# Optimization experiments

Measured on AMD Instinct MI355X. Metric: run time of the kernel, lower is better.

## Reference

```python
import jax, jax.numpy as jnp
import numpy as np

IMG_SIZE = 640
NUM_CLASSES = 80
KA = 3
STRIDES = (8, 16, 32)
CONF_THRESH = 0.001
NMS_THRESH = 0.6
ANCHORS = np.array([[12, 16], [19, 36], [40, 28],
                    [36, 75], [76, 55], [72, 146],
                    [142, 110], [192, 243], [459, 401]], np.float32).reshape(3, 3, 2)
CLS_OFFSET = 4.0  # > max normalized coord (1.0); separates classes for class-wise NMS


def _make_grid(stride):
    f = IMG_SIZE // stride
    gy, gx = jnp.meshgrid(jnp.arange(f), jnp.arange(f), indexing='ij')
    # [HW, 1, 2] in (x, y) order, row-major over (H, W) like permute(1,2,0).view(-1,...)
    return jnp.stack([gx, gy], axis=-1).reshape(-1, 1, 2).astype(jnp.float32)


def _decode_level(pred, level):
    # pred: [KA*(1+C+4), H, W] -> obj [HW*KA,1], cls [HW*KA,C], boxes [HW*KA,4]
    C = NUM_CLASSES
    p = jnp.transpose(pred, (1, 2, 0)).reshape(-1, KA * (1 + C + 4))  # [HW, ch]
    obj = p[:, :KA].reshape(-1, 1)
    cls = p[:, KA:KA * (1 + C)].reshape(-1, C)
    reg = p[:, KA * (1 + C):].reshape(-1, KA, 4)
    grid = _make_grid(STRIDES[level])               # [HW, 1, 2]
    anchors = jnp.asarray(ANCHORS[level])           # [KA, 2]
    xy = (jax.nn.sigmoid(reg[..., :2]) + grid) * STRIDES[level]
    wh = jnp.exp(reg[..., 2:]) * anchors
    box = jnp.concatenate([xy - wh * 0.5, xy + wh * 0.5], axis=-1).reshape(-1, 4)
    return obj, cls, box


def _greedy_nms(boxes, scores, valid, thresh):
    # Faithful sequential greedy NMS (same math as the numpy loop), via lax.scan.
    N = boxes.shape[0]
    order = jnp.argsort(-scores)
    b = boxes[order]
    v = valid[order]
    areas = (b[:, 2] - b[:, 0]) * (b[:, 3] - b[:, 1])
    idx = jnp.arange(N)

    def step(suppressed, i):
        keep_i = v[i] & jnp.logical_not(suppressed[i])
        xx1 = jnp.maximum(b[i, 0], b[:, 0])
        yy1 = jnp.maximum(b[i, 1], b[:, 1])
        xx2 = jnp.minimum(b[i, 2], b[:, 2])
        yy2 = jnp.minimum(b[i, 3], b[:, 3])
        w = jnp.maximum(1e-28, xx2 - xx1)
        h = jnp.maximum(1e-28, yy2 - yy1)
        inter = w * h
        ovr = inter / (areas[i] + areas - inter + 1e-14)
        suppressed = suppressed | (keep_i & (ovr > thresh) & (idx > i))
        return suppressed, keep_i

    _, kept_sorted = jax.lax.scan(step, jnp.zeros(N, bool), idx)
    return jnp.zeros(N, bool).at[order].set(kept_sorted)


def _forward(pred_s, pred_m, pred_l):
    outs = [_decode_level(p, i) for i, p in enumerate((pred_s, pred_m, pred_l))]
    obj = jnp.concatenate([o[0] for o in outs], axis=0)   # [N, 1]
    cls = jnp.concatenate([o[1] for o in outs], axis=0)   # [N, C]
    box = jnp.concatenate([o[2] for o in outs], axis=0)   # [N, 4]
    bboxes = jnp.clip(box / IMG_SIZE, 0.0, 1.0)
    scores = jax.nn.sigmoid(obj) * jax.nn.softmax(cls, axis=-1)  # [N, C]
    cls_inds = jnp.argmax(scores, axis=1)
    conf = jnp.max(scores, axis=1)
    valid = conf >= CONF_THRESH
    # per-class NMS == class-offset trick: different classes never overlap
    nms_boxes = bboxes + cls_inds.astype(bboxes.dtype)[:, None] * CLS_OFFSET
    keep = _greedy_nms(jax.lax.stop_gradient(nms_boxes),
                       jax.lax.stop_gradient(conf), valid, NMS_THRESH)
    return bboxes, conf, cls_inds, keep


def setup_inputs() -> dict:
    key = jax.random.key(0)
    k1, k2, k3 = jax.random.split(key, 3)
    ch = KA * (1 + NUM_CLASSES + 4)  # 255
    return {
        'pred_s': jax.random.normal(k1, (ch, 80, 80), jnp.float32),
        'pred_m': jax.random.normal(k2, (ch, 40, 40), jnp.float32),
        'pred_l': jax.random.normal(k3, (ch, 20, 20), jnp.float32),
    }


def reference(pred_s, pred_m, pred_l):
    # returns fixed-shape (bboxes [N,4], scores [N], cls_inds [N], keep mask [N])
    return _forward(pred_s, pred_m, pred_l)
```

## Files before the change

### kernel.cpp

```cpp
#include <hip/hip_runtime.h>

typedef unsigned long long u64;
typedef unsigned int u32;

#define N_TOT 25200
#define NCLS 80
#define CAP 512

__device__ __constant__ float c_AW[9] = {12.f,19.f,40.f,36.f,76.f,72.f,142.f,192.f,459.f};
__device__ __constant__ float c_AH[9] = {16.f,36.f,28.f,75.f,55.f,146.f,110.f,243.f,401.f};

__global__ __launch_bounds__(64)
void decode_kernel(const float* __restrict__ p0,
                   const float* __restrict__ p1,
                   const float* __restrict__ p2,
                   float* __restrict__ out)
{
    const int m = blockIdx.x * 64 + threadIdx.x;
    if (m >= N_TOT) return;

    const float* p; int f, strd, base, ml;
    int lvl;
    if (m < 19200)      { p = p0; f = 80; strd = 8;  base = 0;     lvl = 0; ml = m; }
    else if (m < 24000) { p = p1; f = 40; strd = 16; base = 19200; lvl = 1; ml = m - 19200; }
    else                { p = p2; f = 20; strd = 32; base = 24000; lvl = 2; ml = m - 24000; }
    const int HW = f * f;
    const int a  = ml / HW;
    const int hw = ml - a * HW;
    const int gx = hw % f;
    const int gy = hw / f;
    const float* cell = p + hw;

    const float* clsp = cell + (3 + a * NCLS) * HW;
    float v[80];
    #pragma unroll
    for (int c = 0; c < 80; ++c) v[c] = clsp[c * HW];
    const float obj = cell[a * HW];
    const float* regp = cell + (243 + a * 4) * HW;
    const float tx = regp[0];
    const float ty = regp[HW];
    const float tw = regp[2 * HW];
    const float th = regp[3 * HW];

    float gm = v[0];
    #pragma unroll
    for (int c = 1; c < 80; ++c) gm = fmaxf(gm, v[c]);
    float gs = 0.f, bp = -1.f; int ba_ = 0;
    #pragma unroll
    for (int c = 0; c < 80; ++c) {
        const float pc = expf(v[c] - gm);
        gs += pc;
        if (pc > bp) { bp = pc; ba_ = c; }
    }

    const float sig  = 1.f / (1.f + expf(-obj));
    const float conf = sig * (bp / gs);
    const int n = base + hw * 3 + a;

    const float sx = 1.f / (1.f + expf(-tx));
    const float sy = 1.f / (1.f + expf(-ty));
    const float cx = (sx + (float)gx) * (float)strd;
    const float cy = (sy + (float)gy) * (float)strd;
    const int ai = lvl * 3 + a;
    const float w  = expf(tw) * c_AW[ai];
    const float h  = expf(th) * c_AH[ai];
    const float hx = w * 0.5f, hy = h * 0.5f;
    float x1 = (cx - hx) / 640.0f;
    float y1 = (cy - hy) / 640.0f;
    float x2 = (cx + hx) / 640.0f;
    float y2 = (cy + hy) / 640.0f;
    x1 = fminf(fmaxf(x1, 0.f), 1.f);
    y1 = fminf(fmaxf(y1, 0.f), 1.f);
    x2 = fminf(fmaxf(x2, 0.f), 1.f);
    y2 = fminf(fmaxf(y2, 0.f), 1.f);

    *(float4*)(out + n * 4) = make_float4(x1, y1, x2, y2);
    out[100800 + n] = conf;
    out[126000 + n] = (float)ba_;
    out[151200 + n] = 0.0f;
}

__global__ __launch_bounds__(1024)
void nms_kernel(const float* __restrict__ out,
                float* __restrict__ out_keep)
{
    const int c = blockIdx.x;
    const int tid = threadIdx.x;
    const int wave = tid >> 6, lane = tid & 63;

    __shared__ int    scnt;
    __shared__ u64    skey[CAP];
    __shared__ float4 sbox[CAP + 1];
    __shared__ int    sgi[CAP];
    __shared__ u64    maskT[8 * CAP];

    if (tid == 0) scnt = 0;
    __syncthreads();

    const float* confp = out + 100800;
    const float* clsp  = out + 126000;
    float4 cf[7], cl[7];
    bool   inb[7];
    #pragma unroll
    for (int itr = 0; itr < 7; ++itr) {
        const int ib = itr * 1024 + tid;
        inb[itr] = (ib < 6300);
        if (inb[itr]) {
            cf[itr] = *(const float4*)(confp + ib * 4);
            cl[itr] = *(const float4*)(clsp  + ib * 4);
        } else {
            cf[itr] = make_float4(-1.f, -1.f, -1.f, -1.f);
            cl[itr] = make_float4(0.f, 0.f, 0.f, 0.f);
        }
    }
    const u64 lt = (1ull << lane) - 1ull;
    #pragma unroll
    for (int itr = 0; itr < 7; ++itr) {
        const bool m0 = inb[itr] && ((int)cl[itr].x == c) && (cf[itr].x >= 0.001f);
        const bool m1 = inb[itr] && ((int)cl[itr].y == c) && (cf[itr].y >= 0.001f);
        const bool m2 = inb[itr] && ((int)cl[itr].z == c) && (cf[itr].z >= 0.001f);
        const bool m3 = inb[itr] && ((int)cl[itr].w == c) && (cf[itr].w >= 0.001f);
        const u64 b0 = __ballot(m0), b1 = __ballot(m1), b2 = __ballot(m2), b3 = __ballot(m3);
        const int t0 = __popcll(b0), t1 = __popcll(b1), t2 = __popcll(b2), t3 = __popcll(b3);
        const int tot = t0 + t1 + t2 + t3;
        if (tot) {
            int bs = 0;
            if (lane == 0) bs = atomicAdd(&scnt, tot);
            bs = __shfl(bs, 0);
            const int i0 = itr * 4096 + tid * 4;
            int pos;
            if (m0) { pos = bs + __popcll(b0 & lt);
                      if (pos < CAP) skey[pos] = ((u64)__float_as_uint(cf[itr].x) << 32) | (u64)(~(u32)(i0)); }
            if (m1) { pos = bs + t0 + __popcll(b1 & lt);
                      if (pos < CAP) skey[pos] = ((u64)__float_as_uint(cf[itr].y) << 32) | (u64)(~(u32)(i0 + 1)); }
            if (m2) { pos = bs + t0 + t1 + __popcll(b2 & lt);
                      if (pos < CAP) skey[pos] = ((u64)__float_as_uint(cf[itr].z) << 32) | (u64)(~(u32)(i0 + 2)); }
            if (m3) { pos = bs + t0 + t1 + t2 + __popcll(b3 & lt);
                      if (pos < CAP) skey[pos] = ((u64)__float_as_uint(cf[itr].w) << 32) | (u64)(~(u32)(i0 + 3)); }
        }
    }
    __syncthreads();
    const int M  = min(scnt, CAP);
    const int MW = (M + 63) >> 6;

    if (wave < MW) {
        const int e = (wave << 6) + lane;
        if (e < M) {
            const u64 ke = skey[e];
            int rank = 0;
            int j = 0;
            for (; j + 16 <= M; j += 16) {
                rank += (int)(skey[j]    > ke) + (int)(skey[j+1]  > ke)
                      + (int)(skey[j+2]  > ke) + (int)(skey[j+3]  > ke)
                      + (int)(skey[j+4]  > ke) + (int)(skey[j+5]  > ke)
                      + (int)(skey[j+6]  > ke) + (int)(skey[j+7]  > ke)
                      + (int)(skey[j+8]  > ke) + (int)(skey[j+9]  > ke)
                      + (int)(skey[j+10] > ke) + (int)(skey[j+11] > ke)
                      + (int)(skey[j+12] > ke) + (int)(skey[j+13] > ke)
                      + (int)(skey[j+14] > ke) + (int)(skey[j+15] > ke);
            }
            for (; j < M; ++j) rank += (int)(skey[j] > ke);

            const u32 gi = ~(u32)ke;
            const float4 b = *(const float4*)(out + gi * 4);
            const float off = 4.0f * (float)c;
            sbox[rank] = make_float4(b.x + off, b.y + off, b.z + off, b.w + off);
            sgi[rank]  = (int)gi;
        }
    }
    __syncthreads();

#define IOU_BIT(RB, I) {                                                \
        const float ra = ((RB).z - (RB).x) * ((RB).w - (RB).y);         \
        float xx1 = fmaxf((RB).x, cb.x);                                \
        float yy1 = fmaxf((RB).y, cb.y);                                \
        float xx2 = fminf((RB).z, cb.z);                                \
        float yy2 = fminf((RB).w, cb.w);                                \
        float ww = fmaxf(1e-28f, xx2 - xx1);                            \
        float hh = fmaxf(1e-28f, yy2 - yy1);                            \
        float inter = ww * hh;                                          \
        float ovr = inter / (ra + ca - inter + 1e-14f);                 \
        bits |= (u64)(((I) < j) && (ovr >= 0.6f)) << ((I) & 63);        \
    }
    const int ntiles = (MW * (MW + 1)) >> 1;
    for (int tt = wave; tt < ntiles; tt += 16) {
        int rw = 0, acc = 0;
        while (tt >= acc + (MW - rw)) { acc += MW - rw; ++rw; }
        const int cw = rw + (tt - acc);
        const int j  = (cw << 6) + lane;
        const float4 cb = sbox[min(j, M - 1)];
        const float  ca = (cb.z - cb.x) * (cb.w - cb.y);
        const int r0 = rw << 6;
        const int r1 = min(r0 + 64, M);
        u64 bits = 0ull;
        int i = r0;
        for (; i + 4 <= r1; i += 4) {
            const float4 b0 = sbox[i];
            const float4 b1 = sbox[i + 1];
            const float4 b2 = sbox[i + 2];
            const float4 b3 = sbox[i + 3];
            IOU_BIT(b0, i) IOU_BIT(b1, i + 1) IOU_BIT(b2, i + 2) IOU_BIT(b3, i + 3)
        }
        for (; i < r1; ++i) {
            const float4 b0 = sbox[i];
            IOU_BIT(b0, i)
        }
        maskT[rw * CAP + j] = bits;
    }
#undef IOU_BIT
    __syncthreads();

    if (wave != 0) return;

    u64 k0 = 0, k1 = 0, k2 = 0, k3 = 0, k4 = 0, k5 = 0, k6 = 0, k7 = 0;
    (void)k7;
#define MT(W) maskT[(W) * CAP + j]
#define TILE(W, PRE)                                                    \
    if ((W) < MW) {                                                     \
        const int j = ((W) << 6) + lane;                                \
        const u64 mine = MT(W);                                         \
        const u64 pre = (PRE);                                          \
        const int rm = M - ((W) << 6);                                  \
        const u64 valid = (rm >= 64) ? ~0ull : ((1ull << rm) - 1ull);   \
        u64 cand = valid & ~__ballot(pre != 0ull);                      \
        u64 kept = 0ull;                                                \
        while (cand) {                                                  \
            const u64 remv = cand & __ballot((mine & kept) != 0ull);    \
            cand &= ~remv;                                              \
            const u64 newk = cand & __ballot((mine & cand) == 0ull);    \
            kept |= newk;                                               \
            cand &= ~newk;                                              \
        }                                                               \
        k##W = kept;                                                    \
        if ((kept >> lane) & 1ull) out_keep[sgi[j]] = 1.0f;             \
    }
    TILE(0, 0ull)
    TILE(1, (MT(0)&k0))
    TILE(2, (MT(0)&k0)|(MT(1)&k1))
    TILE(3, (MT(0)&k0)|(MT(1)&k1)|(MT(2)&k2))
    TILE(4, (MT(0)&k0)|(MT(1)&k1)|(MT(2)&k2)|(MT(3)&k3))
    TILE(5, (MT(0)&k0)|(MT(1)&k1)|(MT(2)&k2)|(MT(3)&k3)|(MT(4)&k4))
    TILE(6, (MT(0)&k0)|(MT(1)&k1)|(MT(2)&k2)|(MT(3)&k3)|(MT(4)&k4)|(MT(5)&k5))
    TILE(7, (MT(0)&k0)|(MT(1)&k1)|(MT(2)&k2)|(MT(3)&k3)|(MT(4)&k4)|(MT(5)&k5)|(MT(6)&k6))
#undef TILE
#undef MT
}

extern "C" void kernel_launch(void* const* d_in, const int* in_sizes, int n_in,
                              void* d_out, int out_size, void* d_ws, size_t ws_size,
                              hipStream_t stream) {
    const float* p0 = (const float*)d_in[0];
    const float* p1 = (const float*)d_in[1];
    const float* p2 = (const float*)d_in[2];
    float* out = (float*)d_out;

    decode_kernel<<<(N_TOT + 63) / 64, 64, 0, stream>>>(p0, p1, p2, out);
    nms_kernel<<<NCLS, 1024, 0, stream>>>(out, out + 151200);
}
```

Before: 44.16 us.

## Fuse decode and NMS into one kernel with a global atomic barrier

Merges the decode and per-class NMS kernels into a single 160-block launch. Each block decodes a 160-anchor slice, then all blocks meet at a global atomic counter, and the first 80 blocks wait on it before running class NMS with 512 threads. This removes one kernel launch and the gap between kernels. In exchange, decode parallelism drops from 394 small blocks to 160 blocks using only 160 of 512 threads, a memset is added, and correctness relies on all 160 blocks being resident at once.

```diff
diff --git a/kernel.cpp b/kernel.cpp
--- a/kernel.cpp
+++ b/kernel.cpp
@@ -6,85 +6,20 @@
 #define N_TOT 25200
 #define NCLS 80
 #define CAP 512
+#define NBLK 160
+#define SLICE 160
 
 __device__ __constant__ float c_AW[9] = {12.f,19.f,40.f,36.f,76.f,72.f,142.f,192.f,459.f};
 __device__ __constant__ float c_AH[9] = {16.f,36.f,28.f,75.f,55.f,146.f,110.f,243.f,401.f};
 
-__global__ __launch_bounds__(64)
-void decode_kernel(const float* __restrict__ p0,
-                   const float* __restrict__ p1,
-                   const float* __restrict__ p2,
-                   float* __restrict__ out)
+__global__ __launch_bounds__(512)
+void fused_kernel(const float* __restrict__ p0,
+                  const float* __restrict__ p1,
+                  const float* __restrict__ p2,
+                  u32* __restrict__ bar,
+                  float* out)
 {
-    const int m = blockIdx.x * 64 + threadIdx.x;
-    if (m >= N_TOT) return;
-
-    const float* p; int f, strd, base, ml;
-    int lvl;
-    if (m < 19200)      { p = p0; f = 80; strd = 8;  base = 0;     lvl = 0; ml = m; }
-    else if (m < 24000) { p = p1; f = 40; strd = 16; base = 19200; lvl = 1; ml = m - 19200; }
-    else                { p = p2; f = 20; strd = 32; base = 24000; lvl = 2; ml = m - 24000; }
-    const int HW = f * f;
-    const int a  = ml / HW;
-    const int hw = ml - a * HW;
-    const int gx = hw % f;
-    const int gy = hw / f;
-    const float* cell = p + hw;
-
-    const float* clsp = cell + (3 + a * NCLS) * HW;
-    float v[80];
-    #pragma unroll
-    for (int c = 0; c < 80; ++c) v[c] = clsp[c * HW];
-    const float obj = cell[a * HW];
-    const float* regp = cell + (243 + a * 4) * HW;
-    const float tx = regp[0];
-    const float ty = regp[HW];
-    const float tw = regp[2 * HW];
-    const float th = regp[3 * HW];
-
-    float gm = v[0];
-    #pragma unroll
-    for (int c = 1; c < 80; ++c) gm = fmaxf(gm, v[c]);
-    float gs = 0.f, bp = -1.f; int ba_ = 0;
-    #pragma unroll
-    for (int c = 0; c < 80; ++c) {
-        const float pc = expf(v[c] - gm);
-        gs += pc;
-        if (pc > bp) { bp = pc; ba_ = c; }
-    }
-
-    const float sig  = 1.f / (1.f + expf(-obj));
-    const float conf = sig * (bp / gs);
-    const int n = base + hw * 3 + a;
-
-    const float sx = 1.f / (1.f + expf(-tx));
-    const float sy = 1.f / (1.f + expf(-ty));
-    const float cx = (sx + (float)gx) * (float)strd;
-    const float cy = (sy + (float)gy) * (float)strd;
-    const int ai = lvl * 3 + a;
-    const float w  = expf(tw) * c_AW[ai];
-    const float h  = expf(th) * c_AH[ai];
-    const float hx = w * 0.5f, hy = h * 0.5f;
-    float x1 = (cx - hx) / 640.0f;
-    float y1 = (cy - hy) / 640.0f;
-    float x2 = (cx + hx) / 640.0f;
-    float y2 = (cy + hy) / 640.0f;
-    x1 = fminf(fmaxf(x1, 0.f), 1.f);
-    y1 = fminf(fmaxf(y1, 0.f), 1.f);
-    x2 = fminf(fmaxf(x2, 0.f), 1.f);
-    y2 = fminf(fmaxf(y2, 0.f), 1.f);
-
-    *(float4*)(out + n * 4) = make_float4(x1, y1, x2, y2);
-    out[100800 + n] = conf;
-    out[126000 + n] = (float)ba_;
-    out[151200 + n] = 0.0f;
-}
-
-__global__ __launch_bounds__(1024)
-void nms_kernel(const float* __restrict__ out,
-                float* __restrict__ out_keep)
-{
-    const int c = blockIdx.x;
+    const int bid = blockIdx.x;
     const int tid = threadIdx.x;
     const int wave = tid >> 6, lane = tid & 63;
 
@@ -95,19 +30,94 @@
     __shared__ u64    maskT[8 * CAP];
 
     if (tid == 0) scnt = 0;
-    __syncthreads();
+
+    const int m = bid * SLICE + tid;
+    if (tid < SLICE && m < N_TOT) {
+        const float* p; int f, strd, base, ml, lvl;
+        if (m < 19200)      { p = p0; f = 80; strd = 8;  base = 0;     lvl = 0; ml = m; }
+        else if (m < 24000) { p = p1; f = 40; strd = 16; base = 19200; lvl = 1; ml = m - 19200; }
+        else                { p = p2; f = 20; strd = 32; base = 24000; lvl = 2; ml = m - 24000; }
+        const int HW = f * f;
+        const int a  = ml / HW;
+        const int hw = ml - a * HW;
+        const int gx = hw % f;
+        const int gy = hw / f;
+        const float* cell = p + hw;
+
+        const float* clsp = cell + (3 + a * NCLS) * HW;
+        float v[80];
+        #pragma unroll
+        for (int c = 0; c < 80; ++c) v[c] = clsp[c * HW];
+        const float obj = cell[a * HW];
+        const float* regp = cell + (243 + a * 4) * HW;
+        const float tx = regp[0];
+        const float ty = regp[HW];
+        const float tw = regp[2 * HW];
+        const float th = regp[3 * HW];
+
+        float gm = v[0];
+        #pragma unroll
+        for (int c = 1; c < 80; ++c) gm = fmaxf(gm, v[c]);
+        float gs = 0.f, bp = -1.f; int ba_ = 0;
+        #pragma unroll
+        for (int c = 0; c < 80; ++c) {
+            const float pc = expf(v[c] - gm);
+            gs += pc;
+            if (pc > bp) { bp = pc; ba_ = c; }
+        }
+
+        const float sig  = 1.f / (1.f + expf(-obj));
+        const float conf = sig * (bp / gs);
+        const int n = base + hw * 3 + a;
+
+        const float sx = 1.f / (1.f + expf(-tx));
+        const float sy = 1.f / (1.f + expf(-ty));
+        const float cx = (sx + (float)gx) * (float)strd;
+        const float cy = (sy + (float)gy) * (float)strd;
+        const int ai = lvl * 3 + a;
+        const float w  = expf(tw) * c_AW[ai];
+        const float h  = expf(th) * c_AH[ai];
+        const float hx = w * 0.5f, hy = h * 0.5f;
+        float x1 = (cx - hx) / 640.0f;
+        float y1 = (cy - hy) / 640.0f;
+        float x2 = (cx + hx) / 640.0f;
+        float y2 = (cy + hy) / 640.0f;
+        x1 = fminf(fmaxf(x1, 0.f), 1.f);
+        y1 = fminf(fmaxf(y1, 0.f), 1.f);
+        x2 = fminf(fmaxf(x2, 0.f), 1.f);
+        y2 = fminf(fmaxf(y2, 0.f), 1.f);
+
+        *(float4*)(out + n * 4) = make_float4(x1, y1, x2, y2);
+        out[100800 + n] = conf;
+        out[126000 + n] = (float)ba_;
+        out[151200 + n] = 0.0f;
+    }
+
+    __threadfence();
+    __syncthreads();
+    if (tid == 0) atomicAdd(bar, 1u);
+    if (bid >= NCLS) return;
+
+    if (tid == 0) {
+        while (__hip_atomic_load(bar, __ATOMIC_ACQUIRE, __HIP_MEMORY_SCOPE_AGENT) < NBLK)
+            __builtin_amdgcn_s_sleep(8);
+    }
+    __syncthreads();
+    __threadfence();
+
+    const int c = bid;
 
     const float* confp = out + 100800;
-    const float* clsp  = out + 126000;
-    float4 cf[7], cl[7];
-    bool   inb[7];
+    const float* clsp2 = out + 126000;
+    float4 cf[13], cl[13];
+    bool   inb[13];
     #pragma unroll
-    for (int itr = 0; itr < 7; ++itr) {
-        const int ib = itr * 1024 + tid;
+    for (int itr = 0; itr < 13; ++itr) {
+        const int ib = itr * 512 + tid;
         inb[itr] = (ib < 6300);
         if (inb[itr]) {
             cf[itr] = *(const float4*)(confp + ib * 4);
-            cl[itr] = *(const float4*)(clsp  + ib * 4);
+            cl[itr] = *(const float4*)(clsp2 + ib * 4);
         } else {
             cf[itr] = make_float4(-1.f, -1.f, -1.f, -1.f);
             cl[itr] = make_float4(0.f, 0.f, 0.f, 0.f);
@@ -115,7 +125,7 @@
     }
     const u64 lt = (1ull << lane) - 1ull;
     #pragma unroll
-    for (int itr = 0; itr < 7; ++itr) {
+    for (int itr = 0; itr < 13; ++itr) {
         const bool m0 = inb[itr] && ((int)cl[itr].x == c) && (cf[itr].x >= 0.001f);
         const bool m1 = inb[itr] && ((int)cl[itr].y == c) && (cf[itr].y >= 0.001f);
         const bool m2 = inb[itr] && ((int)cl[itr].z == c) && (cf[itr].z >= 0.001f);
@@ -127,7 +137,7 @@
             int bs = 0;
             if (lane == 0) bs = atomicAdd(&scnt, tot);
             bs = __shfl(bs, 0);
-            const int i0 = itr * 4096 + tid * 4;
+            const int i0 = itr * 2048 + tid * 4;
             int pos;
             if (m0) { pos = bs + __popcll(b0 & lt);
                       if (pos < CAP) skey[pos] = ((u64)__float_as_uint(cf[itr].x) << 32) | (u64)(~(u32)(i0)); }
@@ -183,7 +193,7 @@
         bits |= (u64)(((I) < j) && (ovr >= 0.6f)) << ((I) & 63);        \
     }
     const int ntiles = (MW * (MW + 1)) >> 1;
-    for (int tt = wave; tt < ntiles; tt += 16) {
+    for (int tt = wave; tt < ntiles; tt += 8) {
         int rw = 0, acc = 0;
         while (tt >= acc + (MW - rw)) { acc += MW - rw; ++rw; }
         const int cw = rw + (tt - acc);
@@ -232,7 +242,7 @@
             cand &= ~newk;                                              \
         }                                                               \
         k##W = kept;                                                    \
-        if ((kept >> lane) & 1ull) out_keep[sgi[j]] = 1.0f;             \
+        if ((kept >> lane) & 1ull) out[151200 + sgi[j]] = 1.0f;         \
     }
     TILE(0, 0ull)
     TILE(1, (MT(0)&k0))
@@ -253,7 +263,8 @@
     const float* p1 = (const float*)d_in[1];
     const float* p2 = (const float*)d_in[2];
     float* out = (float*)d_out;
-
-    decode_kernel<<<(N_TOT + 63) / 64, 64, 0, stream>>>(p0, p1, p2, out);
-    nms_kernel<<<NCLS, 1024, 0, stream>>>(out, out + 151200);
+    u32* bar = (u32*)d_ws;
+
+    hipMemsetAsync(bar, 0, sizeof(u32), stream);
+    fused_kernel<<<NBLK, 512, 0, stream>>>(p0, p1, p2, bar, out);
 }
```

Result: slower. 89.16 us (+101.9%).

## Drop rank sort; build full unsorted IoU mask and resolve NMS by fixpoint

Applied to the files above, without the earlier changes.

Removes the O(M^2) rank-counting sort pass and the sync around it by loading boxes straight into shared memory in insertion order. Suppression order now comes from comparing score keys inside the IoU mask, which is built over all MW×MW tiles rather than the upper triangle, with row boxes broadcast by shuffle and readlane. Greedy NMS is then resolved by an iterative fixpoint over all tiles in wave 0 instead of a sequential tile sweep. This roughly doubles mask computation and may take more rounds to converge, but it drops a sort phase and a barrier.

```diff
diff --git a/kernel.cpp b/kernel.cpp
--- a/kernel.cpp
+++ b/kernel.cpp
@@ -9,6 +9,12 @@
 
 __device__ __constant__ float c_AW[9] = {12.f,19.f,40.f,36.f,76.f,72.f,142.f,192.f,459.f};
 __device__ __constant__ float c_AH[9] = {16.f,36.f,28.f,75.f,55.f,146.f,110.f,243.f,401.f};
+
+__device__ __forceinline__ u64 rdlane64(u64 v, int l) {
+    u32 lo = __builtin_amdgcn_readlane((u32)v, l);
+    u32 hi = __builtin_amdgcn_readlane((u32)(v >> 32), l);
+    return ((u64)hi << 32) | (u64)lo;
+}
 
 __global__ __launch_bounds__(64)
 void decode_kernel(const float* __restrict__ p0,
@@ -19,8 +25,7 @@
     const int m = blockIdx.x * 64 + threadIdx.x;
     if (m >= N_TOT) return;
 
-    const float* p; int f, strd, base, ml;
-    int lvl;
+    const float* p; int f, strd, base, ml, lvl;
     if (m < 19200)      { p = p0; f = 80; strd = 8;  base = 0;     lvl = 0; ml = m; }
     else if (m < 24000) { p = p1; f = 40; strd = 16; base = 19200; lvl = 1; ml = m - 19200; }
     else                { p = p2; f = 20; strd = 32; base = 24000; lvl = 2; ml = m - 24000; }
@@ -89,12 +94,14 @@
     const int wave = tid >> 6, lane = tid & 63;
 
     __shared__ int    scnt;
+    __shared__ float4 sbox[CAP];
     __shared__ u64    skey[CAP];
-    __shared__ float4 sbox[CAP + 1];
     __shared__ int    sgi[CAP];
     __shared__ u64    maskT[8 * CAP];
 
     if (tid == 0) scnt = 0;
+    #pragma unroll
+    for (int z = 0; z < 4; ++z) maskT[tid + (z << 10)] = 0ull;
     __syncthreads();
 
     const float* confp = out + 100800;
@@ -105,15 +112,20 @@
     for (int itr = 0; itr < 7; ++itr) {
         const int ib = itr * 1024 + tid;
         inb[itr] = (ib < 6300);
+        cf[itr] = make_float4(-1.f, -1.f, -1.f, -1.f);
+        cl[itr] = make_float4(0.f, 0.f, 0.f, 0.f);
         if (inb[itr]) {
             cf[itr] = *(const float4*)(confp + ib * 4);
             cl[itr] = *(const float4*)(clsp  + ib * 4);
-        } else {
-            cf[itr] = make_float4(-1.f, -1.f, -1.f, -1.f);
-            cl[itr] = make_float4(0.f, 0.f, 0.f, 0.f);
-        }
-    }
+        }
+    }
+    asm volatile("" : "+v"(cf[0].x), "+v"(cf[1].x), "+v"(cf[2].x), "+v"(cf[3].x),
+                      "+v"(cf[4].x), "+v"(cf[5].x), "+v"(cf[6].x),
+                      "+v"(cl[0].x), "+v"(cl[1].x), "+v"(cl[2].x), "+v"(cl[3].x),
+                      "+v"(cl[4].x), "+v"(cl[5].x), "+v"(cl[6].x));
+
     const u64 lt = (1ull << lane) - 1ull;
+    const float off = 4.0f * (float)c;
     #pragma unroll
     for (int itr = 0; itr < 7; ++itr) {
         const bool m0 = inb[itr] && ((int)cl[itr].x == c) && (cf[itr].x >= 0.001f);
@@ -128,122 +140,108 @@
             if (lane == 0) bs = atomicAdd(&scnt, tot);
             bs = __shfl(bs, 0);
             const int i0 = itr * 4096 + tid * 4;
-            int pos;
-            if (m0) { pos = bs + __popcll(b0 & lt);
-                      if (pos < CAP) skey[pos] = ((u64)__float_as_uint(cf[itr].x) << 32) | (u64)(~(u32)(i0)); }
-            if (m1) { pos = bs + t0 + __popcll(b1 & lt);
-                      if (pos < CAP) skey[pos] = ((u64)__float_as_uint(cf[itr].y) << 32) | (u64)(~(u32)(i0 + 1)); }
-            if (m2) { pos = bs + t0 + t1 + __popcll(b2 & lt);
-                      if (pos < CAP) skey[pos] = ((u64)__float_as_uint(cf[itr].z) << 32) | (u64)(~(u32)(i0 + 2)); }
-            if (m3) { pos = bs + t0 + t1 + t2 + __popcll(b3 & lt);
-                      if (pos < CAP) skey[pos] = ((u64)__float_as_uint(cf[itr].w) << 32) | (u64)(~(u32)(i0 + 3)); }
+            if (m0) { const int pos = bs + __popcll(b0 & lt);
+                if (pos < CAP) { const u32 gi = (u32)(i0);
+                    const float4 b = *(const float4*)(out + gi * 4);
+                    sbox[pos] = make_float4(b.x + off, b.y + off, b.z + off, b.w + off);
+                    skey[pos] = ((u64)__float_as_uint(cf[itr].x) << 32) | (u64)(~gi);
+                    sgi[pos]  = (int)gi; } }
+            if (m1) { const int pos = bs + t0 + __popcll(b1 & lt);
+                if (pos < CAP) { const u32 gi = (u32)(i0 + 1);
+                    const float4 b = *(const float4*)(out + gi * 4);
+                    sbox[pos] = make_float4(b.x + off, b.y + off, b.z + off, b.w + off);
+                    skey[pos] = ((u64)__float_as_uint(cf[itr].y) << 32) | (u64)(~gi);
+                    sgi[pos]  = (int)gi; } }
+            if (m2) { const int pos = bs + t0 + t1 + __popcll(b2 & lt);
+                if (pos < CAP) { const u32 gi = (u32)(i0 + 2);
+                    const float4 b = *(const float4*)(out + gi * 4);
+                    sbox[pos] = make_float4(b.x + off, b.y + off, b.z + off, b.w + off);
+                    skey[pos] = ((u64)__float_as_uint(cf[itr].z) << 32) | (u64)(~gi);
+                    sgi[pos]  = (int)gi; } }
+            if (m3) { const int pos = bs + t0 + t1 + t2 + __popcll(b3 & lt);
+                if (pos < CAP) { const u32 gi = (u32)(i0 + 3);
+                    const float4 b = *(const float4*)(out + gi * 4);
+                    sbox[pos] = make_float4(b.x + off, b.y + off, b.z + off, b.w + off);
+                    skey[pos] = ((u64)__float_as_uint(cf[itr].w) << 32) | (u64)(~gi);
+                    sgi[pos]  = (int)gi; } }
         }
     }
     __syncthreads();
     const int M  = min(scnt, CAP);
     const int MW = (M + 63) >> 6;
 
-    if (wave < MW) {
-        const int e = (wave << 6) + lane;
-        if (e < M) {
-            const u64 ke = skey[e];
-            int rank = 0;
-            int j = 0;
-            for (; j + 16 <= M; j += 16) {
-                rank += (int)(skey[j]    > ke) + (int)(skey[j+1]  > ke)
-                      + (int)(skey[j+2]  > ke) + (int)(skey[j+3]  > ke)
-                      + (int)(skey[j+4]  > ke) + (int)(skey[j+5]  > ke)
-                      + (int)(skey[j+6]  > ke) + (int)(skey[j+7]  > ke)
-                      + (int)(skey[j+8]  > ke) + (int)(skey[j+9]  > ke)
-                      + (int)(skey[j+10] > ke) + (int)(skey[j+11] > ke)
-                      + (int)(skey[j+12] > ke) + (int)(skey[j+13] > ke)
-                      + (int)(skey[j+14] > ke) + (int)(skey[j+15] > ke);
-            }
-            for (; j < M; ++j) rank += (int)(skey[j] > ke);
-
-            const u32 gi = ~(u32)ke;
-            const float4 b = *(const float4*)(out + gi * 4);
-            const float off = 4.0f * (float)c;
-            sbox[rank] = make_float4(b.x + off, b.y + off, b.z + off, b.w + off);
-            sgi[rank]  = (int)gi;
-        }
+    const int nt = MW * MW;
+    for (int t = wave; t < nt; t += 16) {
+        const int rwi = t / MW;
+        const int cwi = t - rwi * MW;
+        const int j  = (cwi << 6) + lane;
+        const int jc = min(j, M - 1);
+        const float4 cb = sbox[jc];
+        const u64    ck = skey[jc];
+        const float  ca = (cb.z - cb.x) * (cb.w - cb.y);
+        const int r0 = rwi << 6;
+        const int rl = min(64, M - r0);
+        const int rr = min(r0 + lane, M - 1);
+        const float4 rbl = sbox[rr];
+        const u64    rkl = skey[rr];
+        u64 bits = 0ull;
+        for (int i = 0; i < rl; ++i) {
+            const float rx = __shfl(rbl.x, i);
+            const float ry = __shfl(rbl.y, i);
+            const float rz = __shfl(rbl.z, i);
+            const float rw2 = __shfl(rbl.w, i);
+            const u64   rk = rdlane64(rkl, i);
+            const float ra = (rz - rx) * (rw2 - ry);
+            const float xx1 = fmaxf(rx, cb.x);
+            const float yy1 = fmaxf(ry, cb.y);
+            const float xx2 = fminf(rz, cb.z);
+            const float yy2 = fminf(rw2, cb.w);
+            const float ww = fmaxf(1e-28f, xx2 - xx1);
+            const float hh = fmaxf(1e-28f, yy2 - yy1);
+            const float inter = ww * hh;
+            const float ovr = inter / (ra + ca - inter + 1e-14f);
+            bits |= (u64)((rk > ck) && (ovr >= 0.6f)) << i;
+        }
+        maskT[rwi * CAP + j] = bits;
     }
     __syncthreads();
 
-#define IOU_BIT(RB, I) {                                                \
-        const float ra = ((RB).z - (RB).x) * ((RB).w - (RB).y);         \
-        float xx1 = fmaxf((RB).x, cb.x);                                \
-        float yy1 = fmaxf((RB).y, cb.y);                                \
-        float xx2 = fminf((RB).z, cb.z);                                \
-        float yy2 = fminf((RB).w, cb.w);                                \
-        float ww = fmaxf(1e-28f, xx2 - xx1);                            \
-        float hh = fmaxf(1e-28f, yy2 - yy1);                            \
-        float inter = ww * hh;                                          \
-        float ovr = inter / (ra + ca - inter + 1e-14f);                 \
-        bits |= (u64)(((I) < j) && (ovr >= 0.6f)) << ((I) & 63);        \
-    }
-    const int ntiles = (MW * (MW + 1)) >> 1;
-    for (int tt = wave; tt < ntiles; tt += 16) {
-        int rw = 0, acc = 0;
-        while (tt >= acc + (MW - rw)) { acc += MW - rw; ++rw; }
-        const int cw = rw + (tt - acc);
-        const int j  = (cw << 6) + lane;
-        const float4 cb = sbox[min(j, M - 1)];
-        const float  ca = (cb.z - cb.x) * (cb.w - cb.y);
-        const int r0 = rw << 6;
-        const int r1 = min(r0 + 64, M);
-        u64 bits = 0ull;
-        int i = r0;
-        for (; i + 4 <= r1; i += 4) {
-            const float4 b0 = sbox[i];
-            const float4 b1 = sbox[i + 1];
-            const float4 b2 = sbox[i + 2];
-            const float4 b3 = sbox[i + 3];
-            IOU_BIT(b0, i) IOU_BIT(b1, i + 1) IOU_BIT(b2, i + 2) IOU_BIT(b3, i + 3)
-        }
-        for (; i < r1; ++i) {
-            const float4 b0 = sbox[i];
-            IOU_BIT(b0, i)
-        }
-        maskT[rw * CAP + j] = bits;
-    }
-#undef IOU_BIT
-    __syncthreads();
-
     if (wave != 0) return;
 
-    u64 k0 = 0, k1 = 0, k2 = 0, k3 = 0, k4 = 0, k5 = 0, k6 = 0, k7 = 0;
-    (void)k7;
-#define MT(W) maskT[(W) * CAP + j]
-#define TILE(W, PRE)                                                    \
-    if ((W) < MW) {                                                     \
-        const int j = ((W) << 6) + lane;                                \
-        const u64 mine = MT(W);                                         \
-        const u64 pre = (PRE);                                          \
-        const int rm = M - ((W) << 6);                                  \
-        const u64 valid = (rm >= 64) ? ~0ull : ((1ull << rm) - 1ull);   \
-        u64 cand = valid & ~__ballot(pre != 0ull);                      \
-        u64 kept = 0ull;                                                \
-        while (cand) {                                                  \
-            const u64 remv = cand & __ballot((mine & kept) != 0ull);    \
-            cand &= ~remv;                                              \
-            const u64 newk = cand & __ballot((mine & cand) == 0ull);    \
-            kept |= newk;                                               \
-            cand &= ~newk;                                              \
-        }                                                               \
-        k##W = kept;                                                    \
-        if ((kept >> lane) & 1ull) out_keep[sgi[j]] = 1.0f;             \
-    }
-    TILE(0, 0ull)
-    TILE(1, (MT(0)&k0))
-    TILE(2, (MT(0)&k0)|(MT(1)&k1))
-    TILE(3, (MT(0)&k0)|(MT(1)&k1)|(MT(2)&k2))
-    TILE(4, (MT(0)&k0)|(MT(1)&k1)|(MT(2)&k2)|(MT(3)&k3))
-    TILE(5, (MT(0)&k0)|(MT(1)&k1)|(MT(2)&k2)|(MT(3)&k3)|(MT(4)&k4))
-    TILE(6, (MT(0)&k0)|(MT(1)&k1)|(MT(2)&k2)|(MT(3)&k3)|(MT(4)&k4)|(MT(5)&k5))
-    TILE(7, (MT(0)&k0)|(MT(1)&k1)|(MT(2)&k2)|(MT(3)&k3)|(MT(4)&k4)|(MT(5)&k5)|(MT(6)&k6))
-#undef TILE
-#undef MT
+    u64 k0=0,k1=0,k2=0,k3=0,k4=0,k5=0,k6=0,k7=0;
+    u64 c0=0,c1=0,c2=0,c3=0,c4=0,c5=0,c6=0,c7=0;
+#define INITC(W) if ((W) < MW) { const int rm = M - ((W) << 6);               \
+        c##W = (rm >= 64) ? ~0ull : ((1ull << rm) - 1ull); }
+    INITC(0) INITC(1) INITC(2) INITC(3) INITC(4) INITC(5) INITC(6) INITC(7)
+#undef INITC
+    bool changed = true;
+    for (int round = 0; round < 512 && changed; ++round) {
+        changed = false;
+#define STEP(W)                                                                \
+        if ((W) < MW) {                                                        \
+            const int j = ((W) << 6) + lane;                                   \
+            const u64 m0 = maskT[0*CAP+j], m1 = maskT[1*CAP+j];                \
+            const u64 m2 = maskT[2*CAP+j], m3 = maskT[3*CAP+j];                \
+            const u64 m4 = maskT[4*CAP+j], m5 = maskT[5*CAP+j];                \
+            const u64 m6 = maskT[6*CAP+j], m7 = maskT[7*CAP+j];                \
+            const u64 preK = (m0&k0)|(m1&k1)|(m2&k2)|(m3&k3)                   \
+                           | (m4&k4)|(m5&k5)|(m6&k6)|(m7&k7);                  \
+            const u64 preC = (m0&c0)|(m1&c1)|(m2&c2)|(m3&c3)                   \
+                           | (m4&c4)|(m5&c5)|(m6&c6)|(m7&c7);                  \
+            const bool live = (c##W >> lane) & 1ull;                           \
+            const u64 rem = __ballot(live && (preK != 0ull));                  \
+            const u64 nk  = __ballot(live && (preK == 0ull) && (preC == 0ull));\
+            if (rem | nk) changed = true;                                      \
+            c##W &= ~(rem | nk);                                               \
+            k##W |= nk;                                                        \
+        }
+        STEP(0) STEP(1) STEP(2) STEP(3) STEP(4) STEP(5) STEP(6) STEP(7)
+#undef STEP
+    }
+#define WRITEK(W) if ((W) < MW) { const int j = ((W) << 6) + lane;             \
+        if ((k##W >> lane) & 1ull) out_keep[sgi[j]] = 1.0f; }
+    WRITEK(0) WRITEK(1) WRITEK(2) WRITEK(3) WRITEK(4) WRITEK(5) WRITEK(6) WRITEK(7)
+#undef WRITEK
 }
 
 extern "C" void kernel_launch(void* const* d_in, const int* in_sizes, int n_in,
```

New measurement: 65.01 us. 47.2% more time.
